# Kernel tuning notes

Hardware: AMD Instinct MI355X
Metric: run time of the kernel (lower is better)

Reference implementation:

```python
import jax, jax.numpy as jnp
import numpy as np

D_MODEL = 1024
N_HEADS = 16
D_K = D_MODEL // N_HEADS
BATCH = 8
SEQ = 1024
ROPE_BASE = 10000.0


def setup_inputs() -> dict:
    key = jax.random.key(0)
    ks = jax.random.split(key, 9)
    s = 1.0 / np.sqrt(D_MODEL)
    return {
        "x": jax.random.normal(ks[0], (BATCH, SEQ, D_MODEL), dtype=jnp.float32),
        "position_ids": jnp.arange(SEQ, dtype=jnp.int32)[None, :],
        "Wq": jax.random.normal(ks[1], (D_MODEL, D_MODEL), dtype=jnp.float32) * s,
        "bq": jnp.zeros((D_MODEL,), dtype=jnp.float32),
        "Wk": jax.random.normal(ks[2], (D_MODEL, D_MODEL), dtype=jnp.float32) * s,
        "bk": jnp.zeros((D_MODEL,), dtype=jnp.float32),
        "Wv": jax.random.normal(ks[3], (D_MODEL, D_MODEL), dtype=jnp.float32) * s,
        "bv": jnp.zeros((D_MODEL,), dtype=jnp.float32),
        "Wo": jax.random.normal(ks[4], (D_MODEL, D_MODEL), dtype=jnp.float32) * s,
        "bo": jnp.zeros((D_MODEL,), dtype=jnp.float32),
    }


def _apply_rope(t, position_ids):
    # t: [B, H, S, D_K]; position_ids: [1, S] (broadcast over batch)
    half = D_K // 2
    inv_freq = 1.0 / (ROPE_BASE ** (jnp.arange(half, dtype=jnp.float32) * 2.0 / D_K))
    ang = position_ids.astype(jnp.float32)[..., None] * inv_freq  # [1, S, half]
    cos = jnp.cos(ang)[:, None, :, :]  # [1, 1, S, half]
    sin = jnp.sin(ang)[:, None, :, :]
    t1, t2 = jnp.split(t, 2, axis=-1)
    return jnp.concatenate([t1 * cos - t2 * sin, t1 * sin + t2 * cos], axis=-1)


def reference(x, position_ids, Wq, bq, Wk, bk, Wv, bv, Wo, bo):
    B, S, D = x.shape
    def proj(W, b):
        # torch Linear: x @ W.T + b
        y = jnp.einsum('bsd,ed->bse', x, W) + b
        return y.reshape(B, S, N_HEADS, D_K).transpose(0, 2, 1, 3)  # [B,H,S,Dk]
    Q = proj(Wq, bq)
    K = proj(Wk, bk)
    V = proj(Wv, bv)
    Q = _apply_rope(Q, position_ids)
    K = _apply_rope(K, position_ids)
    scores = jnp.einsum('bhqd,bhkd->bhqk', Q, K) / jnp.sqrt(jnp.float32(D_K))
    attn = jax.nn.softmax(scores, axis=-1)
    out = jnp.einsum('bhqk,bhkd->bhqd', attn, V)
    out = out.transpose(0, 2, 1, 3).reshape(B, S, D)
    return jnp.einsum('bsd,ed->bse', out, Wo) + bo
```

## Files before the change

kernel.cpp:

```cpp
#include <hip/hip_runtime.h>
#include <hip/hip_bf16.h>


typedef __bf16 bf16_t;
typedef __bf16 bf16x8 __attribute__((ext_vector_type(8)));
typedef float  f32x4  __attribute__((ext_vector_type(4)));

static __device__ __forceinline__ f32x4 mfma16(bf16x8 a, bf16x8 b, f32x4 c) {
  return __builtin_amdgcn_mfma_f32_16x16x32_bf16(a, b, c, 0, 0, 0);
}

#if __has_builtin(__builtin_amdgcn_exp2f)
#define EXP2F(x) __builtin_amdgcn_exp2f(x)
#else
#define EXP2F(x) exp2f(x)
#endif

__global__ void k_cast_xf(const float* __restrict__ x, bf16_t* __restrict__ Xf) {
  int g = blockIdx.x * 256 + threadIdx.x;
  int rg = g >> 11, kt = (g >> 6) & 31, lane = g & 63;
  int m = rg * 16 + (lane & 15);
  int k = kt * 32 + (lane >> 4) * 8;
  const float* s = x + (size_t)m * 1024 + k;
  float4 v0 = *(const float4*)s;
  float4 v1 = *(const float4*)(s + 4);
  union { bf16_t b[8]; } pk;
  pk.b[0] = (bf16_t)v0.x; pk.b[1] = (bf16_t)v0.y; pk.b[2] = (bf16_t)v0.z; pk.b[3] = (bf16_t)v0.w;
  pk.b[4] = (bf16_t)v1.x; pk.b[5] = (bf16_t)v1.y; pk.b[6] = (bf16_t)v1.z; pk.b[7] = (bf16_t)v1.w;
  __builtin_memcpy(Xf + (size_t)g * 8, pk.b, 16);
}

__global__ void k_cast_wf(const float* __restrict__ Wq, const float* __restrict__ Wk,
                          const float* __restrict__ Wv, const float* __restrict__ Wo,
                          bf16_t* __restrict__ Wf) {
  int g = blockIdx.x * 256 + threadIdx.x;
  int rg = g >> 11, kt = (g >> 6) & 31, lane = g & 63;
  const float* src = (rg < 64) ? Wq : (rg < 128) ? Wk : (rg < 192) ? Wv : Wo;
  int row = (rg & 63) * 16 + (lane & 15);
  int k = kt * 32 + (lane >> 4) * 8;
  const float* s = src + (size_t)row * 1024 + k;
  float4 v0 = *(const float4*)s;
  float4 v1 = *(const float4*)(s + 4);
  union { bf16_t b[8]; } pk;
  pk.b[0] = (bf16_t)v0.x; pk.b[1] = (bf16_t)v0.y; pk.b[2] = (bf16_t)v0.z; pk.b[3] = (bf16_t)v0.w;
  pk.b[4] = (bf16_t)v1.x; pk.b[5] = (bf16_t)v1.y; pk.b[6] = (bf16_t)v1.z; pk.b[7] = (bf16_t)v1.w;
  __builtin_memcpy(Wf + (size_t)g * 8, pk.b, 16);
}

__global__ void k_rope_table(const int* __restrict__ pos, float2* __restrict__ rt) {
  int s = blockIdx.x * 8 + (threadIdx.x >> 5);
  int f = threadIdx.x & 31;
  float p = (float)pos[s];
  float inv = powf(10000.0f, -(float)(2 * f) / 64.0f);
  float a = p * inv;
  rt[s * 32 + f] = make_float2(cosf(a), sinf(a));
}

#define GEMM_DIRECT_BODY(AfBase, BfBase)                                       \
  const int t = threadIdx.x;                                                   \
  const int lane = t & 63, w = t >> 6;                                         \
  const int hi = lane >> 4, c = lane & 15;                                     \
  const int wm = w >> 2, wn = w & 3;                                           \
  const bf16_t* Ab = (AfBase) + (size_t)((i0 >> 4) + wm * 4) * 16384 + lane * 8; \
  const bf16_t* Bb = (BfBase) + (size_t)((e0 >> 4) + wn * 4) * 16384 + lane * 8; \
  bf16x8 pa0, pa1, pa2, pa3, pb0, pb1, pb2, pb3;                               \
  bf16x8 qa0, qa1, qa2, qa3, qb0, qb1, qb2, qb3;                               \
  f32x4 acc[4][4] = {};                                                        \
  auto loadP = [&](int kt) {                                                   \
    pa0 = *(const bf16x8*)(Ab + kt * 512);                                     \
    pa1 = *(const bf16x8*)(Ab + 16384 + kt * 512);                             \
    pa2 = *(const bf16x8*)(Ab + 32768 + kt * 512);                             \
    pa3 = *(const bf16x8*)(Ab + 49152 + kt * 512);                             \
    pb0 = *(const bf16x8*)(Bb + kt * 512);                                     \
    pb1 = *(const bf16x8*)(Bb + 16384 + kt * 512);                             \
    pb2 = *(const bf16x8*)(Bb + 32768 + kt * 512);                             \
    pb3 = *(const bf16x8*)(Bb + 49152 + kt * 512);                             \
  };                                                                           \
  auto loadQ = [&](int kt) {                                                   \
    qa0 = *(const bf16x8*)(Ab + kt * 512);                                     \
    qa1 = *(const bf16x8*)(Ab + 16384 + kt * 512);                             \
    qa2 = *(const bf16x8*)(Ab + 32768 + kt * 512);                             \
    qa3 = *(const bf16x8*)(Ab + 49152 + kt * 512);                             \
    qb0 = *(const bf16x8*)(Bb + kt * 512);                                     \
    qb1 = *(const bf16x8*)(Bb + 16384 + kt * 512);                             \
    qb2 = *(const bf16x8*)(Bb + 32768 + kt * 512);                             \
    qb3 = *(const bf16x8*)(Bb + 49152 + kt * 512);                             \
  };                                                                           \
  auto compP = [&]() {                                                         \
    bf16x8 a_[4] = {pa0, pa1, pa2, pa3}, b_[4] = {pb0, pb1, pb2, pb3};         \
    _Pragma("unroll") for (int fr = 0; fr < 4; ++fr)                           \
      _Pragma("unroll") for (int nc = 0; nc < 4; ++nc)                         \
        acc[fr][nc] = mfma16(a_[fr], b_[nc], acc[fr][nc]);                     \
  };                                                                           \
  auto compQ = [&]() {                                                         \
    bf16x8 a_[4] = {qa0, qa1, qa2, qa3}, b_[4] = {qb0, qb1, qb2, qb3};         \
    _Pragma("unroll") for (int fr = 0; fr < 4; ++fr)                           \
      _Pragma("unroll") for (int nc = 0; nc < 4; ++nc)                         \
        acc[fr][nc] = mfma16(a_[fr], b_[nc], acc[fr][nc]);                     \
  };                                                                           \
  loadP(0);                                                                    \
  loadQ(1);                                                                    \
  _Pragma("unroll 3")                                                          \
  for (int jj = 0; jj < 15; ++jj) {                                            \
    compP(); loadP(jj * 2 + 2);                                                \
    compQ(); loadQ(jj * 2 + 3);                                                \
  }                                                                            \
  compP();                                                                     \
  compQ();

__global__ __launch_bounds__(512) void k_gemm_qkv(
    const bf16_t* __restrict__ Xf, const bf16_t* __restrict__ Wf,
    const float* __restrict__ bq, const float* __restrict__ bk,
    const float* __restrict__ bv, const float2* __restrict__ rt,
    bf16_t* __restrict__ Qh, bf16_t* __restrict__ Kg, bf16_t* __restrict__ Vg) {
  const int bid = blockIdx.x;
  const int x = bid & 7, q = bid >> 3;
  const int i0 = (x * 8 + (q & 7)) * 128;
  const int e0 = (q >> 3) * 256;

  GEMM_DIRECT_BODY(Xf, Wf)

  const int z = e0 >> 10;
  const int ez0 = (e0 & 1023) + wn * 64;
  const int h = ez0 >> 6;
  const float* bias = (z == 0) ? bq : (z == 1) ? bk : bv;
  if (z == 2) {
#pragma unroll
    for (int fr = 0; fr < 4; ++fr) {
      int i = i0 + wm * 64 + fr * 16 + hi * 4;
      int b_ = i >> 10, sbase = i & 1023;
      int bhv = b_ * 16 + h;
      int lane_ = c | (((sbase >> 3) & 3) << 4);
#pragma unroll
      for (int nc = 0; nc < 4; ++nc) {
        float bv_ = bias[ez0 + nc * 16 + c];
        union { bf16_t b[4]; } pk;
#pragma unroll
        for (int r = 0; r < 4; ++r) pk.b[r] = (bf16_t)(acc[fr][nc][r] + bv_);
        size_t g = (size_t)(bhv * 4 + nc) * 32 + (sbase >> 5);
        __builtin_memcpy(&Vg[g * 512 + lane_ * 8 + (sbase & 7)], pk.b, 8);
      }
    }
  } else if (z == 0) {
    const float scl = 0.18033688011112042f;
#pragma unroll
    for (int fr = 0; fr < 4; ++fr) {
      int i = i0 + wm * 64 + fr * 16 + hi * 4;
      int b_ = i >> 10, sbase = i & 1023;
      size_t obase = (size_t)((b_ * 16 + h) * 1024);
#pragma unroll
      for (int nc = 0; nc < 2; ++nc) {
        int f = nc * 16 + c;
        float b1_ = bias[ez0 + f], b2_ = bias[ez0 + f + 32];
#pragma unroll
        for (int r = 0; r < 4; ++r) {
          int s = sbase + r;
          float2 cs = rt[s * 32 + f];
          float q1 = acc[fr][nc][r] + b1_;
          float q2 = acc[fr][nc + 2][r] + b2_;
          Qh[(obase + s) * 64 + f] = (bf16_t)((q1 * cs.x - q2 * cs.y) * scl);
          Qh[(obase + s) * 64 + f + 32] = (bf16_t)((q1 * cs.y + q2 * cs.x) * scl);
        }
      }
    }
  } else {
#pragma unroll
    for (int fr = 0; fr < 4; ++fr) {
      int i = i0 + wm * 64 + fr * 16 + hi * 4;
      int b_ = i >> 10, sbase = i & 1023;
      bf16_t* gb = Kg + (size_t)((b_ * 16 + h) * 64 + (sbase >> 4)) * 1024;
#pragma unroll
      for (int nc = 0; nc < 2; ++nc) {
        int f = nc * 16 + c;
        float b1_ = bias[ez0 + f], b2_ = bias[ez0 + f + 32];
        int laneHi = (nc * 2 + (c >> 3)) << 4;
#pragma unroll
        for (int r = 0; r < 4; ++r) {
          int s = sbase + r;
          float2 cs = rt[s * 32 + f];
          float q1 = acc[fr][nc][r] + b1_;
          float q2 = acc[fr][nc + 2][r] + b2_;
          size_t off = (size_t)((hi * 4 + r) | laneHi) * 8 + (c & 7);
          gb[off] = (bf16_t)(q1 * cs.x - q2 * cs.y);
          gb[off + 512] = (bf16_t)(q1 * cs.y + q2 * cs.x);
        }
      }
    }
  }
}

__global__ __launch_bounds__(512) void k_gemm_out(
    const bf16_t* __restrict__ Ogf, const bf16_t* __restrict__ Wf,
    const float* __restrict__ bo, float* __restrict__ out) {
  const int bid = blockIdx.x;
  const int x = bid & 7, q = bid >> 3;
  const int i0 = (x * 8 + (q & 7)) * 128;
  const int e0 = (q >> 3) * 256;
  const bf16_t* WfO = Wf + (size_t)192 * 16384;

  GEMM_DIRECT_BODY(Ogf, WfO)

#pragma unroll
  for (int fr = 0; fr < 4; ++fr) {
    int i = i0 + wm * 64 + fr * 16 + hi * 4;
#pragma unroll
    for (int nc = 0; nc < 4; ++nc) {
      int e = e0 + wn * 64 + nc * 16 + c;
      float bv_ = bo[e];
#pragma unroll
      for (int r = 0; r < 4; ++r)
        out[(size_t)(i + r) * 1024 + e] = acc[fr][nc][r] + bv_;
    }
  }
}

__global__ __launch_bounds__(512) void k_attn(
    const bf16_t* __restrict__ Qh, const bf16_t* __restrict__ Kg,
    const bf16_t* __restrict__ Vg, bf16_t* __restrict__ Ogf) {
  __shared__ alignas(16) char PL[8][2048];
  const int t = threadIdx.x;
  const int lane = t & 63, w = t >> 6;
  const int hi = lane >> 4, c = lane & 15;
  const int bid = blockIdx.x;
  const int wg = (bid & 7) * 64 + (bid >> 3);
  const int bh = wg >> 2, qt = wg & 3;
  const int q0 = qt * 256 + w * 32;
  const size_t qbase = (size_t)bh * 64 * 1024;

  const bf16_t* Kb = Kg + (size_t)bh * 65536 + lane * 8;
  const bf16_t* Vb = Vg + (size_t)bh * 65536 + lane * 8;

  bf16x8 qfA[2], qfB[2];
#pragma unroll
  for (int kk = 0; kk < 2; ++kk) {
    qfA[kk] = *(const bf16x8*)&Qh[qbase + (size_t)(q0 + c) * 64 + kk * 32 + hi * 8];
    qfB[kk] = *(const bf16x8*)&Qh[qbase + (size_t)(q0 + 16 + c) * 64 + kk * 32 + hi * 8];
  }

  f32x4 oA[4] = {}, oB[4] = {};
  float mA = -1e30f, lA = 0.f, mB = -1e30f, lB = 0.f;
  char* const plw = &PL[w][0];

  bf16x8 kp[8], kq[8], vv[8];
#pragma unroll
  for (int ni = 0; ni < 4; ++ni)
#pragma unroll
    for (int kk = 0; kk < 2; ++kk)
      kp[ni * 2 + kk] = *(const bf16x8*)(Kb + (ni * 2 + kk) * 512);

#define SM_PV(ST, M, L, O)                                                     \
  {                                                                            \
    float pmax = -1e30f;                                                       \
    _Pragma("unroll") for (int ni = 0; ni < 4; ++ni)                           \
      _Pragma("unroll") for (int r = 0; r < 4; ++r)                            \
        pmax = fmaxf(pmax, ST[ni][r]);                                         \
    pmax = fmaxf(pmax, __shfl_xor(pmax, 16));                                  \
    pmax = fmaxf(pmax, __shfl_xor(pmax, 32));                                  \
    float mn = fmaxf(M, pmax);                                                 \
    float scale = EXP2F(M - mn);                                               \
    M = mn;                                                                    \
    float psum = 0.f;                                                          \
    _Pragma("unroll") for (int ni = 0; ni < 4; ++ni) {                         \
      union { bf16_t b[4]; } pk;                                               \
      _Pragma("unroll") for (int r = 0; r < 4; ++r) {                          \
        float p = EXP2F(ST[ni][r] - mn);                                       \
        psum += p;                                                             \
        pk.b[r] = (bf16_t)p;                                                   \
      }                                                                        \
      __builtin_memcpy(plw + (ni * 2 + (hi >> 1)) * 256 + c * 16 + (hi & 1) * 8, \
                       pk.b, 8);                                               \
    }                                                                          \
    psum += __shfl_xor(psum, 16);                                              \
    psum += __shfl_xor(psum, 32);                                              \
    L = L * scale + psum;                                                      \
    _Pragma("unroll") for (int od = 0; od < 4; ++od)                           \
      _Pragma("unroll") for (int r = 0; r < 4; ++r) O[od][r] *= scale;         \
    bf16x8 pa[2];                                                              \
    __builtin_memcpy(&pa[0], plw + lane * 16, 16);                             \
    __builtin_memcpy(&pa[1], plw + 1024 + lane * 16, 16);                      \
    _Pragma("unroll") for (int od = 0; od < 4; ++od)                           \
      _Pragma("unroll") for (int kk = 0; kk < 2; ++kk)                         \
        O[od] = mfma16(vv[od * 2 + kk], pa[kk], O[od]);                        \
  }

#define ATTN_TILE(KS, KN, KT)                                                  \
  {                                                                            \
    _Pragma("unroll") for (int od = 0; od < 4; ++od)                           \
      _Pragma("unroll") for (int kk = 0; kk < 2; ++kk)                         \
        vv[od * 2 + kk] = *(const bf16x8*)(Vb + (od * 32 + (KT) * 2 + kk) * 512); \
    f32x4 stA[4] = {}, stB[4] = {};                                            \
    _Pragma("unroll") for (int ni = 0; ni < 4; ++ni)                           \
      _Pragma("unroll") for (int kk = 0; kk < 2; ++kk)                         \
        stA[ni] = mfma16(KS[ni * 2 + kk], qfA[kk], stA[ni]);                   \
    _Pragma("unroll") for (int ni = 0; ni < 4; ++ni)                           \
      _Pragma("unroll") for (int kk = 0; kk < 2; ++kk)                         \
        stB[ni] = mfma16(KS[ni * 2 + kk], qfB[kk], stB[ni]);                   \
    if ((KT) + 1 < 16) {                                                       \
      _Pragma("unroll") for (int ni = 0; ni < 4; ++ni)                         \
        _Pragma("unroll") for (int kk = 0; kk < 2; ++kk)                       \
          KN[ni * 2 + kk] =                                                    \
              *(const bf16x8*)(Kb + (((KT) + 1) * 8 + ni * 2 + kk) * 512);     \
    }                                                                          \
    SM_PV(stA, mA, lA, oA)                                                     \
    SM_PV(stB, mB, lB, oB)                                                     \
  }

  for (int jj = 0; jj < 8; ++jj) {
    ATTN_TILE(kp, kq, jj * 2);
    ATTN_TILE(kq, kp, jj * 2 + 1);
  }
#undef ATTN_TILE
#undef SM_PV

  int b_ = bh >> 4, h = bh & 15;
  float ivA = 1.f / lA, ivB = 1.f / lB;
  int rgA = ((b_ << 10) + q0) >> 4;
#pragma unroll
  for (int od = 0; od < 4; ++od) {
    union { bf16_t b[4]; } pk;
#pragma unroll
    for (int r = 0; r < 4; ++r) pk.b[r] = (bf16_t)(oA[od][r] * ivA);
    int kt2 = (h << 1) + (od >> 1);
    int lp = ((od & 1) * 2 + (hi >> 1)) * 16 + c;
    int el = (hi & 1) * 4;
    __builtin_memcpy(&Ogf[((size_t)(rgA * 32 + kt2) * 64 + lp) * 8 + el], pk.b, 8);
  }
  int rgB = rgA + 1;
#pragma unroll
  for (int od = 0; od < 4; ++od) {
    union { bf16_t b[4]; } pk;
#pragma unroll
    for (int r = 0; r < 4; ++r) pk.b[r] = (bf16_t)(oB[od][r] * ivB);
    int kt2 = (h << 1) + (od >> 1);
    int lp = ((od & 1) * 2 + (hi >> 1)) * 16 + c;
    int el = (hi & 1) * 4;
    __builtin_memcpy(&Ogf[((size_t)(rgB * 32 + kt2) * 64 + lp) * 8 + el], pk.b, 8);
  }
}

extern "C" void kernel_launch(void* const* d_in, const int* in_sizes, int n_in,
                              void* d_out, int out_size, void* d_ws, size_t ws_size,
                              hipStream_t stream) {
  const float* x = (const float*)d_in[0];
  const int* pos = (const int*)d_in[1];
  const float* Wq = (const float*)d_in[2];
  const float* bq = (const float*)d_in[3];
  const float* Wk = (const float*)d_in[4];
  const float* bk = (const float*)d_in[5];
  const float* Wv = (const float*)d_in[6];
  const float* bv = (const float*)d_in[7];
  const float* Wo = (const float*)d_in[8];
  const float* bo = (const float*)d_in[9];
  float* out = (float*)d_out;

  char* ws = (char*)d_ws;
  bf16_t* Xf = (bf16_t*)ws;
  bf16_t* Wf = (bf16_t*)(ws + (16u << 20));
  bf16_t* Vg = (bf16_t*)(ws + (24u << 20));
  float2* rt = (float2*)(ws + (42u << 20));
  bf16_t* Qh = (bf16_t*)d_out;
  bf16_t* Kg = (bf16_t*)d_out + (size_t)8 * 1024 * 1024;
  bf16_t* Ogf = Xf;

  k_cast_xf<<<4096, 256, 0, stream>>>(x, Xf);
  k_cast_wf<<<2048, 256, 0, stream>>>(Wq, Wk, Wv, Wo, Wf);
  k_rope_table<<<128, 256, 0, stream>>>(pos, rt);

  k_gemm_qkv<<<768, 512, 0, stream>>>(Xf, Wf, bq, bk, bv, rt, Qh, Kg, Vg);
  k_attn<<<512, 512, 0, stream>>>(Qh, Kg, Vg, Ogf);
  k_gemm_out<<<256, 512, 0, stream>>>(Ogf, Wf, bo, out);
}
```

Baseline: 164.3 us.

## Fuse prep kernels, raise GEMM MFMA priority, widen attention query tile per wave

The three preprocessing kernels (x cast, weight cast, RoPE table) are merged into one launch, which removes launch gaps. The GEMM inner MFMA blocks are wrapped in s_setprio so matrix work gets scheduling priority over loads. The attention kernel now gives each wave 64 queries (four 16-row sub-tiles) instead of 32 and launches half as many blocks, so each K/V fragment load is reused across more queries. The cost is higher register pressure and only 256 blocks, which may underfill the 256 CUs and lower occupancy.

```diff
diff --git a/kernel.cpp b/kernel.cpp
--- a/kernel.cpp
+++ b/kernel.cpp
@@ -16,44 +16,47 @@
 #define EXP2F(x) exp2f(x)
 #endif
 
-__global__ void k_cast_xf(const float* __restrict__ x, bf16_t* __restrict__ Xf) {
-  int g = blockIdx.x * 256 + threadIdx.x;
-  int rg = g >> 11, kt = (g >> 6) & 31, lane = g & 63;
-  int m = rg * 16 + (lane & 15);
-  int k = kt * 32 + (lane >> 4) * 8;
-  const float* s = x + (size_t)m * 1024 + k;
-  float4 v0 = *(const float4*)s;
-  float4 v1 = *(const float4*)(s + 4);
-  union { bf16_t b[8]; } pk;
-  pk.b[0] = (bf16_t)v0.x; pk.b[1] = (bf16_t)v0.y; pk.b[2] = (bf16_t)v0.z; pk.b[3] = (bf16_t)v0.w;
-  pk.b[4] = (bf16_t)v1.x; pk.b[5] = (bf16_t)v1.y; pk.b[6] = (bf16_t)v1.z; pk.b[7] = (bf16_t)v1.w;
-  __builtin_memcpy(Xf + (size_t)g * 8, pk.b, 16);
-}
-
-__global__ void k_cast_wf(const float* __restrict__ Wq, const float* __restrict__ Wk,
-                          const float* __restrict__ Wv, const float* __restrict__ Wo,
-                          bf16_t* __restrict__ Wf) {
-  int g = blockIdx.x * 256 + threadIdx.x;
-  int rg = g >> 11, kt = (g >> 6) & 31, lane = g & 63;
-  const float* src = (rg < 64) ? Wq : (rg < 128) ? Wk : (rg < 192) ? Wv : Wo;
-  int row = (rg & 63) * 16 + (lane & 15);
-  int k = kt * 32 + (lane >> 4) * 8;
-  const float* s = src + (size_t)row * 1024 + k;
-  float4 v0 = *(const float4*)s;
-  float4 v1 = *(const float4*)(s + 4);
-  union { bf16_t b[8]; } pk;
-  pk.b[0] = (bf16_t)v0.x; pk.b[1] = (bf16_t)v0.y; pk.b[2] = (bf16_t)v0.z; pk.b[3] = (bf16_t)v0.w;
-  pk.b[4] = (bf16_t)v1.x; pk.b[5] = (bf16_t)v1.y; pk.b[6] = (bf16_t)v1.z; pk.b[7] = (bf16_t)v1.w;
-  __builtin_memcpy(Wf + (size_t)g * 8, pk.b, 16);
-}
-
-__global__ void k_rope_table(const int* __restrict__ pos, float2* __restrict__ rt) {
-  int s = blockIdx.x * 8 + (threadIdx.x >> 5);
-  int f = threadIdx.x & 31;
-  float p = (float)pos[s];
-  float inv = powf(10000.0f, -(float)(2 * f) / 64.0f);
-  float a = p * inv;
-  rt[s * 32 + f] = make_float2(cosf(a), sinf(a));
+__global__ void k_prep(const float* __restrict__ x, const float* __restrict__ Wq,
+                       const float* __restrict__ Wk, const float* __restrict__ Wv,
+                       const float* __restrict__ Wo, const int* __restrict__ pos,
+                       bf16_t* __restrict__ Xf, bf16_t* __restrict__ Wf,
+                       float2* __restrict__ rt) {
+  const int bid = blockIdx.x;
+  const int t = threadIdx.x;
+  if (bid < 4096) {
+    int g = bid * 256 + t;
+    int rg = g >> 11, kt = (g >> 6) & 31, lane = g & 63;
+    int m = rg * 16 + (lane & 15);
+    int k = kt * 32 + (lane >> 4) * 8;
+    const float* s = x + (size_t)m * 1024 + k;
+    float4 v0 = *(const float4*)s;
+    float4 v1 = *(const float4*)(s + 4);
+    union { bf16_t b[8]; } pk;
+    pk.b[0] = (bf16_t)v0.x; pk.b[1] = (bf16_t)v0.y; pk.b[2] = (bf16_t)v0.z; pk.b[3] = (bf16_t)v0.w;
+    pk.b[4] = (bf16_t)v1.x; pk.b[5] = (bf16_t)v1.y; pk.b[6] = (bf16_t)v1.z; pk.b[7] = (bf16_t)v1.w;
+    __builtin_memcpy(Xf + (size_t)g * 8, pk.b, 16);
+  } else if (bid < 6144) {
+    int g = (bid - 4096) * 256 + t;
+    int rg = g >> 11, kt = (g >> 6) & 31, lane = g & 63;
+    const float* src = (rg < 64) ? Wq : (rg < 128) ? Wk : (rg < 192) ? Wv : Wo;
+    int row = (rg & 63) * 16 + (lane & 15);
+    int k = kt * 32 + (lane >> 4) * 8;
+    const float* s = src + (size_t)row * 1024 + k;
+    float4 v0 = *(const float4*)s;
+    float4 v1 = *(const float4*)(s + 4);
+    union { bf16_t b[8]; } pk;
+    pk.b[0] = (bf16_t)v0.x; pk.b[1] = (bf16_t)v0.y; pk.b[2] = (bf16_t)v0.z; pk.b[3] = (bf16_t)v0.w;
+    pk.b[4] = (bf16_t)v1.x; pk.b[5] = (bf16_t)v1.y; pk.b[6] = (bf16_t)v1.z; pk.b[7] = (bf16_t)v1.w;
+    __builtin_memcpy(Wf + (size_t)g * 8, pk.b, 16);
+  } else {
+    int rb = bid - 6144;
+    int s = rb * 8 + (t >> 5);
+    int f = t & 31;
+    float p = (float)pos[s];
+    float inv = powf(10000.0f, -(float)(2 * f) / 64.0f);
+    float a = p * inv;
+    rt[s * 32 + f] = make_float2(cosf(a), sinf(a));
+  }
 }
 
 #define GEMM_DIRECT_BODY(AfBase, BfBase)                                       \
@@ -88,15 +91,19 @@
   };                                                                           \
   auto compP = [&]() {                                                         \
     bf16x8 a_[4] = {pa0, pa1, pa2, pa3}, b_[4] = {pb0, pb1, pb2, pb3};         \
+    __builtin_amdgcn_s_setprio(1);                                             \
     _Pragma("unroll") for (int fr = 0; fr < 4; ++fr)                           \
       _Pragma("unroll") for (int nc = 0; nc < 4; ++nc)                         \
         acc[fr][nc] = mfma16(a_[fr], b_[nc], acc[fr][nc]);                     \
+    __builtin_amdgcn_s_setprio(0);                                             \
   };                                                                           \
   auto compQ = [&]() {                                                         \
     bf16x8 a_[4] = {qa0, qa1, qa2, qa3}, b_[4] = {qb0, qb1, qb2, qb3};         \
+    __builtin_amdgcn_s_setprio(1);                                             \
     _Pragma("unroll") for (int fr = 0; fr < 4; ++fr)                           \
       _Pragma("unroll") for (int nc = 0; nc < 4; ++nc)                         \
         acc[fr][nc] = mfma16(a_[fr], b_[nc], acc[fr][nc]);                     \
+    __builtin_amdgcn_s_setprio(0);                                             \
   };                                                                           \
   loadP(0);                                                                    \
   loadQ(1);                                                                    \
@@ -222,31 +229,30 @@
   const int lane = t & 63, w = t >> 6;
   const int hi = lane >> 4, c = lane & 15;
   const int bid = blockIdx.x;
-  const int wg = (bid & 7) * 64 + (bid >> 3);
-  const int bh = wg >> 2, qt = wg & 3;
-  const int q0 = qt * 256 + w * 32;
+  const int wg = (bid & 7) * 32 + (bid >> 3);
+  const int bh = wg >> 1, half = wg & 1;
+  const int q0 = half * 512 + w * 64;
   const size_t qbase = (size_t)bh * 64 * 1024;
 
   const bf16_t* Kb = Kg + (size_t)bh * 65536 + lane * 8;
   const bf16_t* Vb = Vg + (size_t)bh * 65536 + lane * 8;
 
-  bf16x8 qfA[2], qfB[2];
-#pragma unroll
-  for (int kk = 0; kk < 2; ++kk) {
-    qfA[kk] = *(const bf16x8*)&Qh[qbase + (size_t)(q0 + c) * 64 + kk * 32 + hi * 8];
-    qfB[kk] = *(const bf16x8*)&Qh[qbase + (size_t)(q0 + 16 + c) * 64 + kk * 32 + hi * 8];
-  }
-
-  f32x4 oA[4] = {}, oB[4] = {};
-  float mA = -1e30f, lA = 0.f, mB = -1e30f, lB = 0.f;
+  bf16x8 qf[4][2];
+#pragma unroll
+  for (int ss = 0; ss < 4; ++ss)
+#pragma unroll
+    for (int kk = 0; kk < 2; ++kk)
+      qf[ss][kk] = *(const bf16x8*)&Qh[qbase + (size_t)(q0 + ss * 16 + c) * 64 +
+                                       kk * 32 + hi * 8];
+
+  f32x4 o[4][4] = {};
+  float m_[4] = {-1e30f, -1e30f, -1e30f, -1e30f};
+  float l_[4] = {0.f, 0.f, 0.f, 0.f};
   char* const plw = &PL[w][0];
 
   bf16x8 kp[8], kq[8], vv[8];
 #pragma unroll
-  for (int ni = 0; ni < 4; ++ni)
-#pragma unroll
-    for (int kk = 0; kk < 2; ++kk)
-      kp[ni * 2 + kk] = *(const bf16x8*)(Kb + (ni * 2 + kk) * 512);
+  for (int i = 0; i < 8; ++i) kp[i] = *(const bf16x8*)(Kb + i * 512);
 
 #define SM_PV(ST, M, L, O)                                                     \
   {                                                                            \
@@ -285,24 +291,19 @@
 
 #define ATTN_TILE(KS, KN, KT)                                                  \
   {                                                                            \
-    _Pragma("unroll") for (int od = 0; od < 4; ++od)                           \
-      _Pragma("unroll") for (int kk = 0; kk < 2; ++kk)                         \
-        vv[od * 2 + kk] = *(const bf16x8*)(Vb + (od * 32 + (KT) * 2 + kk) * 512); \
-    f32x4 stA[4] = {}, stB[4] = {};                                            \
-    _Pragma("unroll") for (int ni = 0; ni < 4; ++ni)                           \
-      _Pragma("unroll") for (int kk = 0; kk < 2; ++kk)                         \
-        stA[ni] = mfma16(KS[ni * 2 + kk], qfA[kk], stA[ni]);                   \
-    _Pragma("unroll") for (int ni = 0; ni < 4; ++ni)                           \
-      _Pragma("unroll") for (int kk = 0; kk < 2; ++kk)                         \
-        stB[ni] = mfma16(KS[ni * 2 + kk], qfB[kk], stB[ni]);                   \
-    if ((KT) + 1 < 16) {                                                       \
+    _Pragma("unroll") for (int i = 0; i < 8; ++i)                              \
+      vv[i] = *(const bf16x8*)(Vb + ((i >> 1) * 32 + (KT) * 2 + (i & 1)) * 512); \
+    _Pragma("unroll") for (int ss = 0; ss < 4; ++ss) {                         \
+      f32x4 st[4] = {};                                                        \
       _Pragma("unroll") for (int ni = 0; ni < 4; ++ni)                         \
         _Pragma("unroll") for (int kk = 0; kk < 2; ++kk)                       \
-          KN[ni * 2 + kk] =                                                    \
-              *(const bf16x8*)(Kb + (((KT) + 1) * 8 + ni * 2 + kk) * 512);     \
+          st[ni] = mfma16(KS[ni * 2 + kk], qf[ss][kk], st[ni]);                \
+      if (ss == 0 && (KT) + 1 < 16) {                                          \
+        _Pragma("unroll") for (int i = 0; i < 8; ++i)                          \
+          KN[i] = *(const bf16x8*)(Kb + (((KT) + 1) * 8 + i) * 512);           \
+      }                                                                        \
+      SM_PV(st, m_[ss], l_[ss], o[ss])                                         \
     }                                                                          \
-    SM_PV(stA, mA, lA, oA)                                                     \
-    SM_PV(stB, mB, lB, oB)                                                     \
   }
 
   for (int jj = 0; jj < 8; ++jj) {
@@ -313,28 +314,21 @@
 #undef SM_PV
 
   int b_ = bh >> 4, h = bh & 15;
-  float ivA = 1.f / lA, ivB = 1.f / lB;
-  int rgA = ((b_ << 10) + q0) >> 4;
-#pragma unroll
-  for (int od = 0; od < 4; ++od) {
-    union { bf16_t b[4]; } pk;
-#pragma unroll
-    for (int r = 0; r < 4; ++r) pk.b[r] = (bf16_t)(oA[od][r] * ivA);
-    int kt2 = (h << 1) + (od >> 1);
-    int lp = ((od & 1) * 2 + (hi >> 1)) * 16 + c;
-    int el = (hi & 1) * 4;
-    __builtin_memcpy(&Ogf[((size_t)(rgA * 32 + kt2) * 64 + lp) * 8 + el], pk.b, 8);
-  }
-  int rgB = rgA + 1;
-#pragma unroll
-  for (int od = 0; od < 4; ++od) {
-    union { bf16_t b[4]; } pk;
-#pragma unroll
-    for (int r = 0; r < 4; ++r) pk.b[r] = (bf16_t)(oB[od][r] * ivB);
-    int kt2 = (h << 1) + (od >> 1);
-    int lp = ((od & 1) * 2 + (hi >> 1)) * 16 + c;
-    int el = (hi & 1) * 4;
-    __builtin_memcpy(&Ogf[((size_t)(rgB * 32 + kt2) * 64 + lp) * 8 + el], pk.b, 8);
+  int rg0 = ((b_ << 10) + q0) >> 4;
+#pragma unroll
+  for (int ss = 0; ss < 4; ++ss) {
+    float iv = 1.f / l_[ss];
+#pragma unroll
+    for (int od = 0; od < 4; ++od) {
+      union { bf16_t b[4]; } pk;
+#pragma unroll
+      for (int r = 0; r < 4; ++r) pk.b[r] = (bf16_t)(o[ss][od][r] * iv);
+      int kt2 = (h << 1) + (od >> 1);
+      int lp = ((od & 1) * 2 + (hi >> 1)) * 16 + c;
+      int el = (hi & 1) * 4;
+      __builtin_memcpy(&Ogf[((size_t)((rg0 + ss) * 32 + kt2) * 64 + lp) * 8 + el],
+                       pk.b, 8);
+    }
   }
 }
 
@@ -362,11 +356,8 @@
   bf16_t* Kg = (bf16_t*)d_out + (size_t)8 * 1024 * 1024;
   bf16_t* Ogf = Xf;
 
-  k_cast_xf<<<4096, 256, 0, stream>>>(x, Xf);
-  k_cast_wf<<<2048, 256, 0, stream>>>(Wq, Wk, Wv, Wo, Wf);
-  k_rope_table<<<128, 256, 0, stream>>>(pos, rt);
-
+  k_prep<<<6272, 256, 0, stream>>>(x, Wq, Wk, Wv, Wo, pos, Xf, Wf, rt);
   k_gemm_qkv<<<768, 512, 0, stream>>>(Xf, Wf, bq, bk, bv, rt, Qh, Kg, Vg);
-  k_attn<<<512, 512, 0, stream>>>(Qh, Kg, Vg, Ogf);
+  k_attn<<<256, 512, 0, stream>>>(Qh, Kg, Vg, Ogf);
   k_gemm_out<<<256, 512, 0, stream>>>(Ogf, Wf, bo, out);
 }
```

Measured after the change: 152.9 us. -6.9%, faster.
